# Kernel tuning notes

Hardware: AMD Instinct MI355X
Metric: run time of the kernel (lower is better)

Reference implementation:

```python
import jax, jax.numpy as jnp
import numpy as np

EPS = 1e-5

def _conv1x1(w, x):
    # w: [out,in], x: [b,in,h,w] -> [b,out,h,w]
    return jnp.einsum('oi,bihw->bohw', w, x)

def _aggregate(resp, persp, t_w, p_w, g_w, z_w, gamma, beta):
    t = _conv1x1(t_w, persp)                      # b,c,h,w
    b, c, h, w = t.shape
    tq = t.reshape(b, c, h * w).transpose(0, 2, 1)            # b,N,c
    p = _conv1x1(p_w, resp).reshape(b, c, -1)                 # b,c,M
    g = _conv1x1(g_w, resp).reshape(b, c, -1).transpose(0, 2, 1)  # b,M,c
    att = jax.nn.softmax(jnp.einsum('bnc,bcm->bnm', tq, p), axis=2)  # b,N,M
    out = jnp.einsum('bnm,bmc->bnc', att, g)                  # b,N,c
    # faithful to torch: .contiguous().view(b,c,h,w) with NO permute
    out = out.reshape(b, c, h, w)
    z = _conv1x1(z_w, out)                                    # b,Cp,h,w
    mean = z.mean(axis=(0, 2, 3), keepdims=True)
    var = z.var(axis=(0, 2, 3), keepdims=True)                # biased (train-mode BN)
    zn = (z - mean) / jnp.sqrt(var + EPS)
    return zn * gamma[None, :, None, None] + beta[None, :, None, None]

def setup_inputs() -> dict:
    key = jax.random.key(0)
    ks = jax.random.split(key, 32)
    Cp, Cr, planes = 256, [64, 256, 512, 1024, 2048], 64
    hw = [48, 48, 24, 12, 6]
    d = {}
    d['perspective'] = jax.random.normal(ks[0], (4, Cp, 48, 48), jnp.float32)
    for i in range(5):
        d[f'response{i}'] = jax.random.normal(ks[1 + i], (4, Cr[i], hw[i], hw[i]), jnp.float32)
    d['t_w'] = jax.random.normal(ks[6], (planes, Cp), jnp.float32) * 0.05
    d['z_w'] = jax.random.normal(ks[7], (Cp, planes), jnp.float32) * 0.05
    for i in range(5):
        d[f'p{i}_w'] = jax.random.normal(ks[8 + 2 * i], (planes, Cr[i]), jnp.float32) * 0.05
        d[f'g{i}_w'] = jax.random.normal(ks[9 + 2 * i], (planes, Cr[i]), jnp.float32) * 0.05
        d[f'bn{i}_g'] = jnp.ones((Cp,), jnp.float32)
        d[f'bn{i}_b'] = jnp.zeros((Cp,), jnp.float32)
    return d

def reference(perspective, response0, response1, response2, response3, response4,
              t_w, z_w,
              p0_w, g0_w, bn0_g, bn0_b,
              p1_w, g1_w, bn1_g, bn1_b,
              p2_w, g2_w, bn2_g, bn2_b,
              p3_w, g3_w, bn3_g, bn3_b,
              p4_w, g4_w, bn4_g, bn4_b):
    resps = [response0, response1, response2, response3, response4]
    ps = [p0_w, p1_w, p2_w, p3_w, p4_w]
    gs = [g0_w, g1_w, g2_w, g3_w, g4_w]
    gms = [bn0_g, bn1_g, bn2_g, bn3_g, bn4_g]
    bts = [bn0_b, bn1_b, bn2_b, bn3_b, bn4_b]
    out = None
    for i in range(5):
        o = _aggregate(resps[i], perspective, t_w, ps[i], gs[i], z_w, gms[i], bts[i])
        out = o if out is None else out + o
    return out
```

## Files before the change

### kernel.cpp

```cpp
#include <hip/hip_runtime.h>
#include <hip/hip_bf16.h>
#include <string.h>

#define BB 4
#define CPc 256
#define NN 2304

typedef __attribute__((ext_vector_type(8))) short bf16x8;
typedef __attribute__((ext_vector_type(4))) float f32x4;

__device__ __forceinline__ short f2b(float x) {
    __hip_bfloat16 h = __float2bfloat16(x);
    return *reinterpret_cast<short*>(&h);
}
__device__ __forceinline__ float b2f16(short v) {
    union { float f; unsigned u; } x;
    x.u = ((unsigned)(unsigned short)v) << 16;
    return x.f;
}

__device__ __forceinline__ void gl2lds16(const void* g, void* l) {
    __builtin_amdgcn_global_load_lds(
        (const __attribute__((address_space(1))) void*)g,
        (__attribute__((address_space(3))) void*)l, 16, 0, 0);
}

__global__ __launch_bounds__(256) void k_wcvt(
    const float* __restrict__ t_w, const float* __restrict__ z_w,
    const float* p0, const float* p1, const float* p2, const float* p3, const float* p4,
    const float* g0, const float* g1, const float* g2, const float* g3, const float* g4,
    short* __restrict__ TWb, short* __restrict__ ZWb,
    short* __restrict__ WPb, short* __restrict__ WGb) {
    int idx = blockIdx.x * 256 + threadIdx.x;
    if (idx < 16384) { TWb[idx] = f2b(t_w[idx]); return; }
    if (idx < 32768) { ZWb[idx - 16384] = f2b(z_w[idx - 16384]); return; }
    int k = idx - 32768;
    bool isP = k < 249856;
    if (!isP) k -= 249856;
    int i, off;
    if (k < 4096)        { i = 0; off = 0; }
    else if (k < 20480)  { i = 1; off = 4096; }
    else if (k < 53248)  { i = 2; off = 20480; }
    else if (k < 118784) { i = 3; off = 53248; }
    else                 { i = 4; off = 118784; }
    const float* s;
    if (isP) s = (i == 0) ? p0 : (i == 1) ? p1 : (i == 2) ? p2 : (i == 3) ? p3 : p4;
    else     s = (i == 0) ? g0 : (i == 1) ? g1 : (i == 2) ? g2 : (i == 3) ? g3 : g4;
    (isP ? WPb : WGb)[k] = f2b(s[k - off]);
}

__global__ __launch_bounds__(256) void k_conv(
    const float* __restrict__ persp,
    const float* r0, const float* r1, const float* r2, const float* r3, const float* r4,
    const short* __restrict__ TWb, const short* __restrict__ WPb, const short* __restrict__ WGb,
    short* __restrict__ TQb, short* __restrict__ PTb, short* __restrict__ GTb,
    float* __restrict__ PPART, float* __restrict__ GPART) {
    const int CUM[7]  = {0, 144, 288, 432, 504, 552, 584};
    const int CRs[6]  = {256, 64, 256, 512, 1024, 2048};
    const int Mus[6]  = {2304, 2304, 2304, 576, 144, 36};
    const int Mps[6]  = {2304, 2304, 2304, 576, 192, 64};
    const int KSs[6]  = {1, 1, 1, 2, 4, 8};
    const int WOFF[6] = {0, 0, 4096, 20480, 53248, 118784};
    const int POFF[6] = {0, 0, 589824, 1179648, 1327104, 1376256};
    const int PBASE[6] = {0, 0, 0, 0, 294912, 491520};

    __shared__ __align__(16) short s_a[2][64][72];

    int blk = blockIdx.x, t = threadIdx.x;
    int w = t >> 6, lane = t & 63, lo = lane & 15, quad = lane >> 4;
    int seg = 0;
#pragma unroll
    for (int s_ = 1; s_ <= 5; ++s_) if (blk >= CUM[s_]) seg = s_;
    int Cr = CRs[seg], M = Mus[seg], Mp = Mps[seg], KS = KSs[seg];
    const float* in = (seg == 0) ? persp : (seg == 1) ? r0 : (seg == 2) ? r1 :
                      (seg == 3) ? r2 : (seg == 4) ? r3 : r4;
    const short* wp = (seg == 0) ? TWb : WPb + WOFF[seg];
    const short* wg = WGb + WOFF[seg];
    bool has_g = (seg != 0);
    int local = blk - CUM[seg];
    int mt = Mp >> 6;
    int b = local / (mt * KS);
    int rem = local % (mt * KS);
    int m0 = (rem / KS) * 64;
    int ksi = rem % KS;
    int kLen = Cr / KS, k0 = ksi * kLen;

    int ml = t & 63;
    int ssw = (ml >> 3) & 7;
    bool mvalid = (m0 + ml) < M;
    const float* inB = in + ((size_t)b * Cr) * M + m0 + ml;

    int mrow = w * 16 + lo;
    int rsw = (mrow >> 3) & 7;

    f32x4 accP[4], accG[4];
#pragma unroll
    for (int ct = 0; ct < 4; ++ct) {
        accP[ct] = f32x4{0.f, 0.f, 0.f, 0.f};
        accG[ct] = f32x4{0.f, 0.f, 0.f, 0.f};
    }

    float pv0[8], pv1[8];
#define LOADCH(KC)                                                              \
    {                                                                           \
        _Pragma("unroll")                                                       \
        for (int r = 0; r < 8; ++r) {                                           \
            int kp = w + r * 4;                                                 \
            pv0[r] = 0.f; pv1[r] = 0.f;                                         \
            if (mvalid) {                                                       \
                pv0[r] = inB[(size_t)((KC) + 2 * kp) * M];                      \
                pv1[r] = inB[(size_t)((KC) + 2 * kp + 1) * M];                  \
            }                                                                   \
        }                                                                       \
    }
#define WRITECH(BUF)                                                            \
    {                                                                           \
        _Pragma("unroll")                                                       \
        for (int r = 0; r < 8; ++r) {                                           \
            int kp = w + r * 4;                                                 \
            int q = kp >> 2, l = kp & 3;                                        \
            short2 pk; pk.x = f2b(pv0[r]); pk.y = f2b(pv1[r]);                  \
            *(short2*)&s_a[BUF][ml][(q ^ ssw) * 8 + l * 2] = pk;                \
        }                                                                       \
    }

    LOADCH(k0);
    WRITECH(0);
    __syncthreads();

    int cur = 0;
    for (int kc = k0; kc < k0 + kLen; kc += 64) {
        bool more = (kc + 64) < (k0 + kLen);
        if (more) LOADCH(kc + 64);

        bf16x8 wf0[4], wf1[4], wg0[4], wg1[4];
#pragma unroll
        for (int ct = 0; ct < 4; ++ct) {
            wf0[ct] = *(const bf16x8*)&wp[(size_t)(ct * 16 + lo) * Cr + kc + quad * 8];
            wf1[ct] = *(const bf16x8*)&wp[(size_t)(ct * 16 + lo) * Cr + kc + 32 + quad * 8];
            if (has_g) {
                wg0[ct] = *(const bf16x8*)&wg[(size_t)(ct * 16 + lo) * Cr + kc + quad * 8];
                wg1[ct] = *(const bf16x8*)&wg[(size_t)(ct * 16 + lo) * Cr + kc + 32 + quad * 8];
            }
        }
        const bf16x8 fr0 = *(const bf16x8*)&s_a[cur][mrow][8 * (quad ^ rsw)];
        const bf16x8 fr1 = *(const bf16x8*)&s_a[cur][mrow][8 * ((4 + quad) ^ rsw)];
#pragma unroll
        for (int ct = 0; ct < 4; ++ct) {
            accP[ct] = __builtin_amdgcn_mfma_f32_16x16x32_bf16(fr0, wf0[ct], accP[ct], 0, 0, 0);
            accP[ct] = __builtin_amdgcn_mfma_f32_16x16x32_bf16(fr1, wf1[ct], accP[ct], 0, 0, 0);
            if (has_g) {
                accG[ct] = __builtin_amdgcn_mfma_f32_16x16x32_bf16(wg0[ct], fr0, accG[ct], 0, 0, 0);
                accG[ct] = __builtin_amdgcn_mfma_f32_16x16x32_bf16(wg1[ct], fr1, accG[ct], 0, 0, 0);
            }
        }
        if (more) WRITECH(cur ^ 1);
        __syncthreads();
        cur ^= 1;
    }
#undef LOADCH
#undef WRITECH

    if (KS == 1) {
        short* outP = (seg == 0) ? TQb : PTb + POFF[seg];
        short* outG = GTb + POFF[seg];
        int mP = m0 + w * 16 + quad * 4;
#pragma unroll
        for (int ct = 0; ct < 4; ++ct) {
            int c = ct * 16 + lo;
#pragma unroll
            for (int rg = 0; rg < 4; ++rg)
                outP[((size_t)b * Mp + mP + rg) * 64 + c] = f2b(accP[ct][rg]);
        }
        if (has_g) {
            int mG = m0 + w * 16 + lo;
#pragma unroll
            for (int ct = 0; ct < 4; ++ct) {
                int cG = ct * 16 + quad * 4;
#pragma unroll
                for (int rg = 0; rg < 4; ++rg)
                    outG[((size_t)b * 64 + cG + rg) * Mp + mG] = f2b(accG[ct][rg]);
            }
        }
    } else {
        int NP = 4 * Mp * 64;
        float* pp = PPART + PBASE[seg] + (size_t)ksi * NP;
        float* gp = GPART + PBASE[seg] + (size_t)ksi * NP;
        int mP = m0 + w * 16 + quad * 4;
#pragma unroll
        for (int ct = 0; ct < 4; ++ct) {
            int c = ct * 16 + lo;
#pragma unroll
            for (int rg = 0; rg < 4; ++rg)
                pp[((size_t)b * Mp + mP + rg) * 64 + c] = accP[ct][rg];
        }
        int mG = m0 + w * 16 + lo;
#pragma unroll
        for (int ct = 0; ct < 4; ++ct) {
            int cG = ct * 16 + quad * 4;
#pragma unroll
            for (int rg = 0; rg < 4; ++rg)
                gp[((size_t)b * 64 + cG + rg) * Mp + mG] = accG[ct][rg];
        }
    }
}

__global__ __launch_bounds__(256) void k_cvt(const float* __restrict__ PPART,
                                             const float* __restrict__ GPART,
                                             short* __restrict__ PTb, short* __restrict__ GTb) {
    const int EC[4]    = {0, 147456, 196608, 212992};
    const int KSv[3]   = {2, 4, 8};
    const int PBASEv[3] = {0, 294912, 491520};
    const int POFFv[3] = {1179648, 1327104, 1376256};
    int e = blockIdx.x * 256 + threadIdx.x;
    int sg = (e < EC[1]) ? 0 : (e < EC[2]) ? 1 : 2;
    int rem = e - EC[sg];
    int KS = KSv[sg];
    int NP = (sg == 0) ? 147456 : (sg == 1) ? 49152 : 16384;
    {
        const float* src = PPART + PBASEv[sg] + rem;
        float p = 0.f;
        for (int s = 0; s < KS; ++s) p += src[(size_t)s * NP];
        PTb[POFFv[sg] + rem] = f2b(p);
    }
    {
        const float* src = GPART + PBASEv[sg] + rem;
        float g = 0.f;
        for (int s = 0; s < KS; ++s) g += src[(size_t)s * NP];
        GTb[POFFv[sg] + rem] = f2b(g);
    }
}

__global__ __launch_bounds__(256) void k_attn(const short* __restrict__ tq,
                                              const short* __restrict__ PTb,
                                              const short* __restrict__ GTb,
                                              short* __restrict__ OUTb,
                                              float* __restrict__ PNUM,
                                              float* __restrict__ PL) {
    const int AM[5]    = {2304, 2304, 576, 144, 36};
    const int AMp[5]   = {2304, 2304, 576, 192, 64};
    const int APOFF[5] = {0, 589824, 1179648, 1327104, 1376256};

    __shared__ __align__(16) short s_tile[2][8192];
    __shared__ __align__(16) short s_P[4][32][72];

    int t = threadIdx.x;
    int bid = blockIdx.x;
    int seg, r, p;
    if (bid < 576) { seg = bid / 288; int wi = bid % 288; p = wi / 72; r = wi % 72; }
    else           { int q = bid - 576; seg = 2 + q / 72; r = q % 72; p = 0; }
    int b = r / 18;
    int n0 = (r % 18) * 128;
    int M = AM[seg], Mp = AMp[seg];
    const short* pT = PTb + APOFF[seg];
    const short* gT = GTb + APOFF[seg];

    int w = t >> 6, lane = t & 63, lo = lane & 15, quad = lane >> 4;
    bool domask = (M != Mp);
    bool split = (seg < 2);
    int n0w = n0 + w * 32;

    int c0, c1;
    if (split) { c0 = p * 9; c1 = c0 + 9; }
    else       { c0 = 0; c1 = Mp >> 6; }

    const short* tqB = tq + ((size_t)b * NN + n0w + lo) * 64 + quad * 8;
    bf16x8 bq[2][2];
#pragma unroll
    for (int i = 0; i < 2; ++i)
#pragma unroll
        for (int h = 0; h < 2; ++h)
            bq[i][h] = *(const bf16x8*)(tqB + i * 16 * 64 + h * 32);

    const short* ptSeg = pT + (size_t)b * Mp * 64;
    const short* gtSeg = gT + (size_t)b * 64 * Mp;

    f32x4 accO[2][4];
#pragma unroll
    for (int i = 0; i < 2; ++i)
#pragma unroll
        for (int cs = 0; cs < 4; ++cs)
            accO[i][cs] = f32x4{0.f, 0.f, 0.f, 0.f};
    float lsum[2] = {0.f, 0.f};

    short (*sp)[72] = s_P[w];

#define STAGE(BUF, M0)                                                          \
    {                                                                           \
        _Pragma("unroll")                                                       \
        for (int j = 0; j < 2; ++j) {                                           \
            int slab = w * 2 + j;                                               \
            int Bb = slab * 1024 + lane * 16;                                   \
            int srcb = Bb ^ (((Bb >> 7) & 7) << 4);                             \
            gl2lds16((const char*)(ptSeg + (size_t)(M0) * 64) + srcb,           \
                     &s_tile[BUF][slab * 512]);                                 \
        }                                                                       \
        _Pragma("unroll")                                                       \
        for (int j = 0; j < 2; ++j) {                                           \
            int slab = w * 2 + j;                                               \
            int row = slab * 8 + (lane >> 3);                                   \
            int colb = (lane & 7) * 16;                                         \
            int colbs = colb ^ ((row & 7) << 4);                                \
            gl2lds16((const char*)(gtSeg + (size_t)row * Mp + (M0)) + colbs,    \
                     &s_tile[BUF][4096 + slab * 512]);                          \
        }                                                                       \
    }

    int buf = 0;
    STAGE(0, c0 << 6);
    __syncthreads();

    int swz = (lo & 7) << 4;
    for (int ch = c0; ch < c1; ++ch) {
        int m0 = ch << 6;
        bool more = (ch + 1 < c1);
        if (more) STAGE(buf ^ 1, m0 + 64);

        const char* ptL = (const char*)&s_tile[buf][0];
        const char* gtL = (const char*)&s_tile[buf][4096];
        bf16x8 pa[4][2], gb[4][2];
#pragma unroll
        for (int ms = 0; ms < 4; ++ms)
#pragma unroll
            for (int h = 0; h < 2; ++h) {
                int A = (ms * 16 + lo) * 128 + h * 64 + quad * 16;
                pa[ms][h] = *(const bf16x8*)(ptL + (A ^ swz));
                gb[ms][h] = *(const bf16x8*)(gtL + (A ^ swz));
            }

        f32x4 S[2][4];
#pragma unroll
        for (int i = 0; i < 2; ++i)
#pragma unroll
            for (int ms = 0; ms < 4; ++ms) {
                S[i][ms] = f32x4{0.f, 0.f, 0.f, 0.f};
                S[i][ms] = __builtin_amdgcn_mfma_f32_16x16x32_bf16(pa[ms][0], bq[i][0], S[i][ms], 0, 0, 0);
                S[i][ms] = __builtin_amdgcn_mfma_f32_16x16x32_bf16(pa[ms][1], bq[i][1], S[i][ms], 0, 0, 0);
            }
        if (domask) {
#pragma unroll
            for (int ms = 0; ms < 4; ++ms)
#pragma unroll
                for (int rg = 0; rg < 4; ++rg) {
                    bool oob = (m0 + ms * 16 + quad * 4 + rg) >= M;
                    if (oob) { S[0][ms][rg] = -1e30f; S[1][ms][rg] = -1e30f; }
                }
        }
#pragma unroll
        for (int i = 0; i < 2; ++i)
#pragma unroll
            for (int ms = 0; ms < 4; ++ms) {
                short4 pw;
#pragma unroll
                for (int rg = 0; rg < 4; ++rg) {
                    float e = __expf(S[i][ms][rg] - 40.f);
                    lsum[i] += e;
                    ((short*)&pw)[rg] = f2b(e);
                }
                *(short4*)&sp[i * 16 + lo][ms * 16 + quad * 4] = pw;
            }
        bf16x8 pf[2][2];
#pragma unroll
        for (int i = 0; i < 2; ++i)
#pragma unroll
            for (int h = 0; h < 2; ++h)
                pf[i][h] = *(const bf16x8*)&sp[i * 16 + lo][h * 32 + quad * 8];
#pragma unroll
        for (int i = 0; i < 2; ++i)
#pragma unroll
            for (int cs = 0; cs < 4; ++cs) {
                accO[i][cs] = __builtin_amdgcn_mfma_f32_16x16x32_bf16(pf[i][0], gb[cs][0], accO[i][cs], 0, 0, 0);
                accO[i][cs] = __builtin_amdgcn_mfma_f32_16x16x32_bf16(pf[i][1], gb[cs][1], accO[i][cs], 0, 0, 0);
            }
        __syncthreads();
        buf ^= 1;
    }
#undef STAGE
#pragma unroll
    for (int i = 0; i < 2; ++i) {
        lsum[i] += __shfl_xor(lsum[i], 16, 64);
        lsum[i] += __shfl_xor(lsum[i], 32, 64);
    }
    if (split) {
        float* np = PNUM + ((size_t)((seg * 4 + p) * 72 + r)) * 8192;
        float* lp = PL + ((size_t)((seg * 4 + p) * 72 + r)) * 128;
        if (quad == 0) {
            lp[w * 32 + lo] = lsum[0];
            lp[w * 32 + 16 + lo] = lsum[1];
        }
#pragma unroll
        for (int i = 0; i < 2; ++i)
#pragma unroll
            for (int cs = 0; cs < 4; ++cs)
#pragma unroll
                for (int rg = 0; rg < 4; ++rg) {
                    int nl = w * 32 + i * 16 + quad * 4 + rg;
                    np[nl * 64 + cs * 16 + lo] = accO[i][cs][rg];
                }
    } else {
        short* outm = OUTb + (size_t)seg * 589824;
#pragma unroll
        for (int i = 0; i < 2; ++i)
#pragma unroll
            for (int rg = 0; rg < 4; ++rg) {
                float lt = __shfl(lsum[i], quad * 4 + rg, 64);
                int n = n0w + i * 16 + quad * 4 + rg;
#pragma unroll
                for (int cs = 0; cs < 4; ++cs)
                    outm[((size_t)b * NN + n) * 64 + cs * 16 + lo] = f2b(accO[i][cs][rg] / lt);
            }
    }
}

__global__ __launch_bounds__(256) void k_comb(const float* __restrict__ PNUM,
                                              const float* __restrict__ PL,
                                              short* __restrict__ OUTb) {
    int e4 = (blockIdx.x * 256 + threadIdx.x) * 4;
    int s = e4 / 589824;
    int rem = e4 % 589824;
    int row = rem / 64;
    int c = rem % 64;
    int b = row / 2304;
    int ng = row % 2304;
    int nblk = ng >> 7;
    int nl = ng & 127;
    int r = b * 18 + nblk;
    float ax = 0.f, ay = 0.f, az = 0.f, aw = 0.f, l = 0.f;
#pragma unroll
    for (int pp = 0; pp < 4; ++pp) {
        size_t base = (size_t)((s * 4 + pp) * 72 + r);
        const float4 v = *(const float4*)&PNUM[base * 8192 + nl * 64 + c];
        ax += v.x; ay += v.y; az += v.z; aw += v.w;
        l += PL[base * 128 + nl];
    }
    short4 o;
    o.x = f2b(ax / l);
    o.y = f2b(ay / l);
    o.z = f2b(az / l);
    o.w = f2b(aw / l);
    *(short4*)&OUTb[e4] = o;
}

__global__ __launch_bounds__(256) void k_z(const short* __restrict__ OUTb,
                                           const short* __restrict__ ZWb,
                                           short* __restrict__ Zb,
                                           float* __restrict__ PART) {
    __shared__ __align__(16) short s_ut[64][72];
    int t = threadIdx.x;
    int seg = blockIdx.x / 144;
    int r = blockIdx.x % 144;
    int b = r / 36;
    int sp0 = (r % 36) * 64;
    const short* F = OUTb + (size_t)seg * 589824 + (size_t)b * 147456;
    short* z = Zb + (size_t)seg * 2359296 + (size_t)b * 589824;
    float* part = PART + (size_t)(seg * 144 + r) * 512;

    int w = t >> 6, lane = t & 63, lo = lane & 15, quad = lane >> 4;

    bf16x8 af[4][2];
#pragma unroll
    for (int qt = 0; qt < 4; ++qt)
#pragma unroll
        for (int h = 0; h < 2; ++h)
            af[qt][h] = *(const bf16x8*)&ZWb[(size_t)(w * 64 + qt * 16 + lo) * 64 + h * 32 + quad * 8];

#pragma unroll
    for (int rr = 0; rr < 4; ++rr) {
        int idx = t + rr * 256;
        int spl = idx & 63;
        int cp0 = (idx >> 6) << 2;
        short4 pk;
        pk.x = F[(size_t)(cp0 + 0) * 2304 + sp0 + spl];
        pk.y = F[(size_t)(cp0 + 1) * 2304 + sp0 + spl];
        pk.z = F[(size_t)(cp0 + 2) * 2304 + sp0 + spl];
        pk.w = F[(size_t)(cp0 + 3) * 2304 + sp0 + spl];
        *(short4*)&s_ut[spl][cp0] = pk;
    }
    __syncthreads();

    bf16x8 bfr[4][2];
#pragma unroll
    for (int st = 0; st < 4; ++st)
#pragma unroll
        for (int h = 0; h < 2; ++h)
            bfr[st][h] = *(const bf16x8*)&s_ut[st * 16 + lo][h * 32 + quad * 8];

    f32x4 acc[4][4];
#pragma unroll
    for (int qt = 0; qt < 4; ++qt)
#pragma unroll
        for (int st = 0; st < 4; ++st) {
            acc[qt][st] = f32x4{0.f, 0.f, 0.f, 0.f};
            acc[qt][st] = __builtin_amdgcn_mfma_f32_16x16x32_bf16(af[qt][0], bfr[st][0], acc[qt][st], 0, 0, 0);
            acc[qt][st] = __builtin_amdgcn_mfma_f32_16x16x32_bf16(af[qt][1], bfr[st][1], acc[qt][st], 0, 0, 0);
        }

#pragma unroll
    for (int qt = 0; qt < 4; ++qt) {
        float s1[4] = {0.f, 0.f, 0.f, 0.f};
        float s2[4] = {0.f, 0.f, 0.f, 0.f};
        int qb = w * 64 + qt * 16 + quad * 4;
#pragma unroll
        for (int st = 0; st < 4; ++st) {
            int sp = sp0 + st * 16 + lo;
#pragma unroll
            for (int rg = 0; rg < 4; ++rg) {
                float v = acc[qt][st][rg];
                z[(size_t)(qb + rg) * 2304 + sp] = f2b(v);
                s1[rg] += v;
                s2[rg] += v * v;
            }
        }
#pragma unroll
        for (int rg = 0; rg < 4; ++rg) {
            for (int o = 8; o >= 1; o >>= 1) {
                s1[rg] += __shfl_xor(s1[rg], o, 16);
                s2[rg] += __shfl_xor(s2[rg], o, 16);
            }
            if (lo == 0) {
                float2 v2; v2.x = s1[rg]; v2.y = s2[rg];
                *(float2*)&part[(size_t)(qb + rg) * 2] = v2;
            }
        }
    }
}

__global__ __launch_bounds__(256) void k_stats(const float* __restrict__ PART,
                                               float* __restrict__ STATS) {
    int seg = blockIdx.x;
    int q = threadIdx.x;
    const float* p = PART + (size_t)seg * 144 * 512 + q * 2;
    float s1 = 0.f, s2 = 0.f;
#pragma unroll 16
    for (int blk = 0; blk < 144; ++blk) {
        float2 v = *(const float2*)&p[(size_t)blk * 512];
        s1 += v.x; s2 += v.y;
    }
    STATS[seg * 512 + q * 2] = s1;
    STATS[seg * 512 + q * 2 + 1] = s2;
}

__global__ __launch_bounds__(256) void k_final(
    const short* __restrict__ Zb, const float* __restrict__ STATS,
    const float* g0, const float* g1, const float* g2, const float* g3, const float* g4,
    const float* b0, const float* b1, const float* b2, const float* b3, const float* b4,
    float* __restrict__ outp) {
    int idx4 = (blockIdx.x * 256 + threadIdx.x) * 4;
    int q = (idx4 / NN) & 255;
    const float inv = 1.f / (float)(BB * NN);
    float4 o = {0.f, 0.f, 0.f, 0.f};
#pragma unroll
    for (int i = 0; i < 5; ++i) {
        float mean = STATS[i * 512 + q * 2] * inv;
        float var = STATS[i * 512 + q * 2 + 1] * inv - mean * mean;
        float rr = rsqrtf(var + 1e-5f);
        const float* gm = (i == 0) ? g0 : (i == 1) ? g1 : (i == 2) ? g2 : (i == 3) ? g3 : g4;
        const float* bt = (i == 0) ? b0 : (i == 1) ? b1 : (i == 2) ? b2 : (i == 3) ? b3 : b4;
        float sc = rr * gm[q];
        float ofs = bt[q] - mean * sc;
        short4 zv = *(const short4*)&Zb[(size_t)i * 2359296 + idx4];
        o.x += b2f16(zv.x) * sc + ofs;
        o.y += b2f16(zv.y) * sc + ofs;
        o.z += b2f16(zv.z) * sc + ofs;
        o.w += b2f16(zv.w) * sc + ofs;
    }
    *(float4*)&outp[idx4] = o;
}

extern "C" void kernel_launch(void* const* d_in, const int* in_sizes, int n_in,
                              void* d_out, int out_size, void* d_ws, size_t ws_size,
                              hipStream_t stream) {
    const float* persp = (const float*)d_in[0];
    const float* resp[5];
    for (int i = 0; i < 5; ++i) resp[i] = (const float*)d_in[1 + i];
    const float* t_w = (const float*)d_in[6];
    const float* z_w = (const float*)d_in[7];
    const float *p_w[5], *g_w[5], *bng[5], *bnb[5];
    for (int i = 0; i < 5; ++i) {
        p_w[i] = (const float*)d_in[8 + 4 * i];
        g_w[i] = (const float*)d_in[9 + 4 * i];
        bng[i] = (const float*)d_in[10 + 4 * i];
        bnb[i] = (const float*)d_in[11 + 4 * i];
    }
    short* TQb = (short*)d_ws;
    short* TWb = TQb + 589824;
    short* ZWb = TWb + 16384;
    short* WPb = ZWb + 16384;
    short* WGb = WPb + 249856;
    short* PTb = WGb + 249856;
    short* GTb = PTb + 1392640;
    short* Zb  = GTb + 1392640;
    short* OUTb  = (short*)((float*)d_ws + 7852032);
    float* STATS = (float*)d_ws + 7852032 + 2949120;
    float* PPART = STATS + 2560;
    float* GPART = PPART + 622592;
    float* PNUM = (float*)Zb;
    float* PL   = PNUM + 4718592;

    k_wcvt<<<2080, 256, 0, stream>>>(t_w, z_w,
        p_w[0], p_w[1], p_w[2], p_w[3], p_w[4],
        g_w[0], g_w[1], g_w[2], g_w[3], g_w[4],
        TWb, ZWb, WPb, WGb);
    k_conv<<<584, 256, 0, stream>>>(persp,
        resp[0], resp[1], resp[2], resp[3], resp[4],
        TWb, WPb, WGb, TQb, PTb, GTb, PPART, GPART);
    k_cvt<<<832, 256, 0, stream>>>(PPART, GPART, PTb, GTb);
    k_attn<<<792, 256, 0, stream>>>(TQb, PTb, GTb, OUTb, PNUM, PL);
    k_comb<<<1152, 256, 0, stream>>>(PNUM, PL, OUTb);
    k_z<<<720, 256, 0, stream>>>(OUTb, ZWb, Zb, PPART);
    k_stats<<<5, 256, 0, stream>>>(PPART, STATS);
    k_final<<<2304, 256, 0, stream>>>(Zb, STATS,
        bng[0], bng[1], bng[2], bng[3], bng[4],
        bnb[0], bnb[1], bnb[2], bnb[3], bnb[4],
        (float*)d_out);
}
```

Before: 221.3 us.

## Fuse weight conversion into conv/z kernels and split-K combine into k_z

Removes the separate weight fp32→bf16 conversion kernel by loading fp32 weights directly in k_conv and k_z and converting in registers. Removes the k_comb kernel by having k_z read the split partial numerators and denominators for segments 0–1 and normalize on the fly while filling shared memory. Workspace is relaid out so PNUM no longer aliases Zb. This saves two launches and an intermediate write/read, at the cost of doubled weight load bytes and strided scalar gathers of PNUM in k_z.

```diff
diff --git a/kernel.cpp b/kernel.cpp
--- a/kernel.cpp
+++ b/kernel.cpp
@@ -19,40 +19,27 @@
     return x.f;
 }
 
+__device__ __forceinline__ bf16x8 ld8cvt(const float* p) {
+    const float4 a = *(const float4*)p;
+    const float4 b = *(const float4*)(p + 4);
+    bf16x8 r;
+    r[0] = f2b(a.x); r[1] = f2b(a.y); r[2] = f2b(a.z); r[3] = f2b(a.w);
+    r[4] = f2b(b.x); r[5] = f2b(b.y); r[6] = f2b(b.z); r[7] = f2b(b.w);
+    return r;
+}
+
 __device__ __forceinline__ void gl2lds16(const void* g, void* l) {
     __builtin_amdgcn_global_load_lds(
         (const __attribute__((address_space(1))) void*)g,
         (__attribute__((address_space(3))) void*)l, 16, 0, 0);
 }
 
-__global__ __launch_bounds__(256) void k_wcvt(
-    const float* __restrict__ t_w, const float* __restrict__ z_w,
-    const float* p0, const float* p1, const float* p2, const float* p3, const float* p4,
-    const float* g0, const float* g1, const float* g2, const float* g3, const float* g4,
-    short* __restrict__ TWb, short* __restrict__ ZWb,
-    short* __restrict__ WPb, short* __restrict__ WGb) {
-    int idx = blockIdx.x * 256 + threadIdx.x;
-    if (idx < 16384) { TWb[idx] = f2b(t_w[idx]); return; }
-    if (idx < 32768) { ZWb[idx - 16384] = f2b(z_w[idx - 16384]); return; }
-    int k = idx - 32768;
-    bool isP = k < 249856;
-    if (!isP) k -= 249856;
-    int i, off;
-    if (k < 4096)        { i = 0; off = 0; }
-    else if (k < 20480)  { i = 1; off = 4096; }
-    else if (k < 53248)  { i = 2; off = 20480; }
-    else if (k < 118784) { i = 3; off = 53248; }
-    else                 { i = 4; off = 118784; }
-    const float* s;
-    if (isP) s = (i == 0) ? p0 : (i == 1) ? p1 : (i == 2) ? p2 : (i == 3) ? p3 : p4;
-    else     s = (i == 0) ? g0 : (i == 1) ? g1 : (i == 2) ? g2 : (i == 3) ? g3 : g4;
-    (isP ? WPb : WGb)[k] = f2b(s[k - off]);
-}
-
 __global__ __launch_bounds__(256) void k_conv(
     const float* __restrict__ persp,
     const float* r0, const float* r1, const float* r2, const float* r3, const float* r4,
-    const short* __restrict__ TWb, const short* __restrict__ WPb, const short* __restrict__ WGb,
+    const float* __restrict__ t_w,
+    const float* p0w, const float* p1w, const float* p2w, const float* p3w, const float* p4w,
+    const float* g0w, const float* g1w, const float* g2w, const float* g3w, const float* g4w,
     short* __restrict__ TQb, short* __restrict__ PTb, short* __restrict__ GTb,
     float* __restrict__ PPART, float* __restrict__ GPART) {
     const int CUM[7]  = {0, 144, 288, 432, 504, 552, 584};
@@ -60,7 +47,6 @@
     const int Mus[6]  = {2304, 2304, 2304, 576, 144, 36};
     const int Mps[6]  = {2304, 2304, 2304, 576, 192, 64};
     const int KSs[6]  = {1, 1, 1, 2, 4, 8};
-    const int WOFF[6] = {0, 0, 4096, 20480, 53248, 118784};
     const int POFF[6] = {0, 0, 589824, 1179648, 1327104, 1376256};
     const int PBASE[6] = {0, 0, 0, 0, 294912, 491520};
 
@@ -74,8 +60,10 @@
     int Cr = CRs[seg], M = Mus[seg], Mp = Mps[seg], KS = KSs[seg];
     const float* in = (seg == 0) ? persp : (seg == 1) ? r0 : (seg == 2) ? r1 :
                       (seg == 3) ? r2 : (seg == 4) ? r3 : r4;
-    const short* wp = (seg == 0) ? TWb : WPb + WOFF[seg];
-    const short* wg = WGb + WOFF[seg];
+    const float* wpf = (seg == 0) ? t_w : (seg == 1) ? p0w : (seg == 2) ? p1w :
+                       (seg == 3) ? p2w : (seg == 4) ? p3w : p4w;
+    const float* wgf = (seg == 1) ? g0w : (seg == 2) ? g1w :
+                       (seg == 3) ? g2w : (seg == 4) ? g3w : g4w;
     bool has_g = (seg != 0);
     int local = blk - CUM[seg];
     int mt = Mp >> 6;
@@ -136,11 +124,11 @@
         bf16x8 wf0[4], wf1[4], wg0[4], wg1[4];
 #pragma unroll
         for (int ct = 0; ct < 4; ++ct) {
-            wf0[ct] = *(const bf16x8*)&wp[(size_t)(ct * 16 + lo) * Cr + kc + quad * 8];
-            wf1[ct] = *(const bf16x8*)&wp[(size_t)(ct * 16 + lo) * Cr + kc + 32 + quad * 8];
+            wf0[ct] = ld8cvt(&wpf[(size_t)(ct * 16 + lo) * Cr + kc + quad * 8]);
+            wf1[ct] = ld8cvt(&wpf[(size_t)(ct * 16 + lo) * Cr + kc + 32 + quad * 8]);
             if (has_g) {
-                wg0[ct] = *(const bf16x8*)&wg[(size_t)(ct * 16 + lo) * Cr + kc + quad * 8];
-                wg1[ct] = *(const bf16x8*)&wg[(size_t)(ct * 16 + lo) * Cr + kc + 32 + quad * 8];
+                wg0[ct] = ld8cvt(&wgf[(size_t)(ct * 16 + lo) * Cr + kc + quad * 8]);
+                wg1[ct] = ld8cvt(&wgf[(size_t)(ct * 16 + lo) * Cr + kc + 32 + quad * 8]);
             }
         }
         const bf16x8 fr0 = *(const bf16x8*)&s_a[cur][mrow][8 * (quad ^ rsw)];
@@ -412,37 +400,10 @@
     }
 }
 
-__global__ __launch_bounds__(256) void k_comb(const float* __restrict__ PNUM,
-                                              const float* __restrict__ PL,
-                                              short* __restrict__ OUTb) {
-    int e4 = (blockIdx.x * 256 + threadIdx.x) * 4;
-    int s = e4 / 589824;
-    int rem = e4 % 589824;
-    int row = rem / 64;
-    int c = rem % 64;
-    int b = row / 2304;
-    int ng = row % 2304;
-    int nblk = ng >> 7;
-    int nl = ng & 127;
-    int r = b * 18 + nblk;
-    float ax = 0.f, ay = 0.f, az = 0.f, aw = 0.f, l = 0.f;
-#pragma unroll
-    for (int pp = 0; pp < 4; ++pp) {
-        size_t base = (size_t)((s * 4 + pp) * 72 + r);
-        const float4 v = *(const float4*)&PNUM[base * 8192 + nl * 64 + c];
-        ax += v.x; ay += v.y; az += v.z; aw += v.w;
-        l += PL[base * 128 + nl];
-    }
-    short4 o;
-    o.x = f2b(ax / l);
-    o.y = f2b(ay / l);
-    o.z = f2b(az / l);
-    o.w = f2b(aw / l);
-    *(short4*)&OUTb[e4] = o;
-}
-
 __global__ __launch_bounds__(256) void k_z(const short* __restrict__ OUTb,
-                                           const short* __restrict__ ZWb,
+                                           const float* __restrict__ z_w,
+                                           const float* __restrict__ PNUM,
+                                           const float* __restrict__ PL,
                                            short* __restrict__ Zb,
                                            float* __restrict__ PART) {
     __shared__ __align__(16) short s_ut[64][72];
@@ -451,7 +412,6 @@
     int r = blockIdx.x % 144;
     int b = r / 36;
     int sp0 = (r % 36) * 64;
-    const short* F = OUTb + (size_t)seg * 589824 + (size_t)b * 147456;
     short* z = Zb + (size_t)seg * 2359296 + (size_t)b * 589824;
     float* part = PART + (size_t)(seg * 144 + r) * 512;
 
@@ -462,19 +422,46 @@
     for (int qt = 0; qt < 4; ++qt)
 #pragma unroll
         for (int h = 0; h < 2; ++h)
-            af[qt][h] = *(const bf16x8*)&ZWb[(size_t)(w * 64 + qt * 16 + lo) * 64 + h * 32 + quad * 8];
-
-#pragma unroll
-    for (int rr = 0; rr < 4; ++rr) {
-        int idx = t + rr * 256;
-        int spl = idx & 63;
-        int cp0 = (idx >> 6) << 2;
-        short4 pk;
-        pk.x = F[(size_t)(cp0 + 0) * 2304 + sp0 + spl];
-        pk.y = F[(size_t)(cp0 + 1) * 2304 + sp0 + spl];
-        pk.z = F[(size_t)(cp0 + 2) * 2304 + sp0 + spl];
-        pk.w = F[(size_t)(cp0 + 3) * 2304 + sp0 + spl];
-        *(short4*)&s_ut[spl][cp0] = pk;
+            af[qt][h] = ld8cvt(&z_w[(size_t)(w * 64 + qt * 16 + lo) * 64 + h * 32 + quad * 8]);
+
+    if (seg < 2) {
+        int sp036 = r % 36;
+#pragma unroll
+        for (int rr = 0; rr < 4; ++rr) {
+            int idx = t + rr * 256;
+            int spl = idx & 63;
+            int cp0 = (idx >> 6) << 2;
+            short4 pk;
+#pragma unroll
+            for (int j = 0; j < 4; ++j) {
+                int ng = (cp0 + j) * 36 + sp036;
+                int rb = b * 18 + (ng >> 7);
+                int nl = ng & 127;
+                float num = 0.f, l = 0.f;
+#pragma unroll
+                for (int pp = 0; pp < 4; ++pp) {
+                    size_t base = (size_t)((seg * 4 + pp) * 72 + rb);
+                    num += PNUM[base * 8192 + nl * 64 + spl];
+                    l   += PL[base * 128 + nl];
+                }
+                ((short*)&pk)[j] = f2b(num / l);
+            }
+            *(short4*)&s_ut[spl][cp0] = pk;
+        }
+    } else {
+        const short* F = OUTb + (size_t)seg * 589824 + (size_t)b * 147456;
+#pragma unroll
+        for (int rr = 0; rr < 4; ++rr) {
+            int idx = t + rr * 256;
+            int spl = idx & 63;
+            int cp0 = (idx >> 6) << 2;
+            short4 pk;
+            pk.x = F[(size_t)(cp0 + 0) * 2304 + sp0 + spl];
+            pk.y = F[(size_t)(cp0 + 1) * 2304 + sp0 + spl];
+            pk.z = F[(size_t)(cp0 + 2) * 2304 + sp0 + spl];
+            pk.w = F[(size_t)(cp0 + 3) * 2304 + sp0 + spl];
+            *(short4*)&s_ut[spl][cp0] = pk;
+        }
     }
     __syncthreads();
 
@@ -582,32 +569,26 @@
         bng[i] = (const float*)d_in[10 + 4 * i];
         bnb[i] = (const float*)d_in[11 + 4 * i];
     }
-    short* TQb = (short*)d_ws;
-    short* TWb = TQb + 589824;
-    short* ZWb = TWb + 16384;
-    short* WPb = ZWb + 16384;
-    short* WGb = WPb + 249856;
-    short* PTb = WGb + 249856;
-    short* GTb = PTb + 1392640;
-    short* Zb  = GTb + 1392640;
-    short* OUTb  = (short*)((float*)d_ws + 7852032);
-    float* STATS = (float*)d_ws + 7852032 + 2949120;
+    short* TQb  = (short*)d_ws;
+    short* PTb  = TQb + 589824;
+    short* GTb  = PTb + 1392640;
+    short* Zb   = GTb + 1392640;
+    short* OUTb = Zb + 11796480;
+    float* STATS = (float*)((short*)d_ws + 18120704);
     float* PPART = STATS + 2560;
     float* GPART = PPART + 622592;
-    float* PNUM = (float*)Zb;
-    float* PL   = PNUM + 4718592;
-
-    k_wcvt<<<2080, 256, 0, stream>>>(t_w, z_w,
+    float* PNUM  = GPART + 622592;
+    float* PL    = PNUM + 4718592;
+
+    k_conv<<<584, 256, 0, stream>>>(persp,
+        resp[0], resp[1], resp[2], resp[3], resp[4],
+        t_w,
         p_w[0], p_w[1], p_w[2], p_w[3], p_w[4],
         g_w[0], g_w[1], g_w[2], g_w[3], g_w[4],
-        TWb, ZWb, WPb, WGb);
-    k_conv<<<584, 256, 0, stream>>>(persp,
-        resp[0], resp[1], resp[2], resp[3], resp[4],
-        TWb, WPb, WGb, TQb, PTb, GTb, PPART, GPART);
+        TQb, PTb, GTb, PPART, GPART);
     k_cvt<<<832, 256, 0, stream>>>(PPART, GPART, PTb, GTb);
     k_attn<<<792, 256, 0, stream>>>(TQb, PTb, GTb, OUTb, PNUM, PL);
-    k_comb<<<1152, 256, 0, stream>>>(PNUM, PL, OUTb);
-    k_z<<<720, 256, 0, stream>>>(OUTb, ZWb, Zb, PPART);
+    k_z<<<720, 256, 0, stream>>>(OUTb, z_w, PNUM, PL, Zb, PPART);
     k_stats<<<5, 256, 0, stream>>>(PPART, STATS);
     k_final<<<2304, 256, 0, stream>>>(Zb, STATS,
         bng[0], bng[1], bng[2], bng[3], bng[4],
```

Result: slower. 228.8 us (+3.4%).
